# Optimization experiments

Measured on AMD Instinct MI355X. Metric: run time of the kernel, lower is better.

The kernel has to match this reference:

```python
import jax, jax.numpy as jnp
import numpy as np

K_NN = 16  # number of nearest neighbors (module init arg k)


def setup_inputs() -> dict:
    key = jax.random.key(0)
    k1, k2 = jax.random.split(key)
    xyz = jax.random.normal(k1, (8, 16384, 3), dtype=jnp.float32)
    centers = jax.random.normal(k2, (8, 1024, 3), dtype=jnp.float32)
    return {"xyz": xyz, "centers": centers}


def reference(xyz, centers):
    # avoiding the (B, N, K, 3) broadcast intermediate of the original while
    # computing the same torch.norm(xyz - centers, dim=-1) math.
    x_sq = jnp.sum(xyz * xyz, axis=-1)          # (B, N)
    c_sq = jnp.sum(centers * centers, axis=-1)  # (B, K)
    cross = jnp.einsum('bnd,bkd->bnk', xyz, centers)  # (B, N, K)
    d2 = x_sq[:, :, None] + c_sq[None if False else slice(None), None, :] - 2.0 * cross
    dist = jnp.sqrt(jnp.maximum(d2, 0.0))       # (B, N, K)
    # torch.topk(dist, k, dim=1, largest=False, sorted=True):
    # smallest-k over the N (points) axis, per center.
    neg = -jnp.transpose(dist, (0, 2, 1))       # (B, K, N)
    _, idx = jax.lax.top_k(neg, K_NN)           # (B, K, k), ascending distance
    return jnp.transpose(idx, (0, 2, 1))        # (B, k, K) to match torch dim=1 topk
```

## Files before the change

kernel.cpp:

```cpp
#include <hip/hip_runtime.h>
#include <stdint.h>

#define BB    8
#define NN    16384
#define KK    1024
#define KNN   16
#define CPB   8
#define WPB   8
#define EGRP  (NN / 4 / WPB)
#define PGRP  128
#define TCAP  256

typedef unsigned long long u64;

__device__ __forceinline__ u64 shfl_xor_u64(u64 v, int mask) {
    int lo = (int)(uint32_t)v;
    int hi = (int)(uint32_t)(v >> 32);
    lo = __shfl_xor(lo, mask, 64);
    hi = __shfl_xor(hi, mask, 64);
    return ((u64)(uint32_t)hi << 32) | (u64)(uint32_t)lo;
}

__device__ __forceinline__ u64 shfl_u64(u64 v, int src) {
    int lo = __shfl((int)(uint32_t)v, src, 64);
    int hi = __shfl((int)(uint32_t)(v >> 32), src, 64);
    return ((u64)(uint32_t)hi << 32) | (u64)(uint32_t)lo;
}

__device__ __forceinline__ u64 wave_min_u64(u64 v) {
#pragma unroll
    for (int off = 32; off > 0; off >>= 1) {
        u64 o = shfl_xor_u64(v, off);
        v = o < v ? o : v;
    }
    return v;
}

__device__ __forceinline__ void sort64_kv(u64& key, uint32_t& pay, int lane) {
#pragma unroll
    for (int k = 2; k <= 64; k <<= 1) {
#pragma unroll
        for (int j = k >> 1; j > 0; j >>= 1) {
            u64 okey = shfl_xor_u64(key, j);
            uint32_t opay = (uint32_t)__shfl_xor((int)pay, j, 64);
            bool tmin = ((lane & j) == 0) == ((lane & k) == 0);
            bool osm = okey < key;
            bool take = tmin ? osm : !osm;
            if (take) { key = okey; pay = opay; }
        }
    }
}

__device__ __forceinline__ void sort64_k(u64& key, int lane) {
#pragma unroll
    for (int k = 2; k <= 64; k <<= 1) {
#pragma unroll
        for (int j = k >> 1; j > 0; j >>= 1) {
            u64 okey = shfl_xor_u64(key, j);
            bool tmin = ((lane & j) == 0) == ((lane & k) == 0);
            bool osm = okey < key;
            bool take = tmin ? osm : !osm;
            if (take) key = okey;
        }
    }
}

__device__ __forceinline__ float point_d2(const float* xb, int i,
                                          float c0, float c1, float c2, float csq) {
#pragma clang fp contract(off)
    float x0 = xb[i * 3 + 0];
    float x1 = xb[i * 3 + 1];
    float x2 = xb[i * 3 + 2];
    float xsq = (x0 * x0 + x1 * x1) + x2 * x2;
    float cross = __fmaf_rn(x2, c2, __fmaf_rn(x1, c1, x0 * c0));
    float d2 = (xsq + csq) - 2.0f * cross;
    return d2 < 0.0f ? 0.0f : d2;
}

__device__ __attribute__((noinline)) int fallback_scan(const float* xb,
                                                       float c0, float c1, float c2,
                                                       float csq, int lane) {
    u64 list[KNN];
#pragma unroll
    for (int j = 0; j < KNN; ++j) list[j] = ~0ull;
    for (int i = lane; i < NN; i += 64) {
        float d2 = point_d2(xb, i, c0, c1, c2, csq);
        float dist = __fsqrt_rn(d2);
        u64 key = ((u64)__float_as_uint(dist) << 32) | (u64)(uint32_t)i;
        if (key < list[KNN - 1]) {
#pragma unroll
            for (int j = 0; j < KNN; ++j) {
                bool lt = key < list[j];
                u64 lo = lt ? key : list[j];
                u64 hi = lt ? list[j] : key;
                list[j] = lo;
                key = hi;
            }
        }
    }
    int res = 0;
    for (int it = 0; it < KNN; ++it) {
        u64 best = wave_min_u64(list[0]);
        if (it == lane) res = (int)(uint32_t)best;
        if (list[0] == best) {
#pragma unroll
            for (int j = 0; j < KNN - 1; ++j) list[j] = list[j + 1];
            list[KNN - 1] = ~0ull;
        }
    }
    return res;
}

__device__ __forceinline__ float sixteenth_smallest(float m, int lane) {
    uint32_t u = __float_as_uint(m);
    uint32_t s = (u & 0x80000000u) ? ~u : (u | 0x80000000u);
    u64 v = ((u64)s << 32) | (unsigned)lane;
#pragma unroll
    for (int k = 2; k <= 64; k <<= 1) {
#pragma unroll
        for (int j = k >> 1; j > 0; j >>= 1) {
            u64 o = shfl_xor_u64(v, j);
            bool up = (lane & k) == 0;
            bool takeMin = ((lane & j) == 0) == up;
            u64 mn = v < o ? v : o;
            u64 mx = v < o ? o : v;
            v = takeMin ? mn : mx;
        }
    }
    uint32_t sb = (uint32_t)__shfl((int)(uint32_t)(v >> 32), 15, 64);
    uint32_t ub = (sb & 0x80000000u) ? (sb ^ 0x80000000u) : ~sb;
    return __uint_as_float(ub);
}

__device__ __forceinline__ void load_group(const float4* x4, int g,
                                           float (&px)[4], float (&py)[4],
                                           float (&pz)[4], float (&xs)[4]) {
#pragma clang fp contract(off)
    float4 f0 = x4[g * 3 + 0];
    float4 f1 = x4[g * 3 + 1];
    float4 f2 = x4[g * 3 + 2];
    px[0] = f0.x; py[0] = f0.y; pz[0] = f0.z;
    px[1] = f0.w; py[1] = f1.x; pz[1] = f1.y;
    px[2] = f1.z; py[2] = f1.w; pz[2] = f2.x;
    px[3] = f2.y; py[3] = f2.z; pz[3] = f2.w;
#pragma unroll
    for (int k = 0; k < 4; ++k)
        xs[k] = (px[k] * px[k] + py[k] * py[k]) + pz[k] * pz[k];
}

__global__ __launch_bounds__(512, 4) void knn_kernel(const float* __restrict__ xyz,
                                                     const float* __restrict__ centers,
                                                     int* __restrict__ out) {
#pragma clang fp contract(off)
    const int q = (int)(threadIdx.x >> 6);
    const int lane = (int)(threadIdx.x & 63);
    const int cbase = (int)blockIdx.x * CPB;
    const int b = cbase >> 10;

    __shared__ float    s_min[CPB][512];
    __shared__ float    s_T[CPB];
    __shared__ int      s_cnt[CPB];
    __shared__ uint32_t s_idx[CPB][TCAP];

    float n[CPB][3];
#pragma unroll
    for (int c = 0; c < CPB; ++c) {
        n[c][0] = -2.0f * centers[(cbase + c) * 3 + 0];
        n[c][1] = -2.0f * centers[(cbase + c) * 3 + 1];
        n[c][2] = -2.0f * centers[(cbase + c) * 3 + 2];
    }

    const float* xb = xyz + (size_t)b * NN * 3;
    const float4* x4 = (const float4*)xb;
    const int gbase = q * EGRP;

    float m[CPB];
#pragma unroll
    for (int c = 0; c < CPB; ++c) m[c] = __builtin_inff();
#pragma unroll
    for (int s = 0; s < PGRP / 64; ++s) {
        int g = gbase + s * 64 + lane;
        float px[4], py[4], pz[4], xs[4];
        load_group(x4, g, px, py, pz, xs);
#pragma unroll
        for (int k = 0; k < 4; ++k) {
#pragma unroll
            for (int c = 0; c < CPB; ++c) {
                float d = __fmaf_rn(px[k], n[c][0],
                          __fmaf_rn(py[k], n[c][1],
                          __fmaf_rn(pz[k], n[c][2], xs[k])));
                m[c] = d < m[c] ? d : m[c];
            }
        }
    }
#pragma unroll
    for (int c = 0; c < CPB; ++c) s_min[c][threadIdx.x] = m[c];
    if (threadIdx.x < CPB) s_cnt[threadIdx.x] = 0;
    __syncthreads();
    {
        float v = s_min[q][lane];
#pragma unroll
        for (int w = 1; w < WPB; ++w) v = fminf(v, s_min[q][w * 64 + lane]);
        float t = sixteenth_smallest(v, lane);
        if (lane == 0) s_T[q] = t;
    }
    __syncthreads();
    float U[CPB];
#pragma unroll
    for (int c = 0; c < CPB; ++c) {
        float T = s_T[c];
        U[c] = T + fabsf(T) * 1e-5f + 5e-4f;
    }

#pragma unroll 2
    for (int s = 0; s < EGRP / 64; ++s) {
        int g = gbase + s * 64 + lane;
        float px[4], py[4], pz[4], xs[4];
        load_group(x4, g, px, py, pz, xs);
#pragma unroll
        for (int k = 0; k < 4; ++k) {
            int i = g * 4 + k;
#pragma unroll
            for (int c = 0; c < CPB; ++c) {
                float d = __fmaf_rn(px[k], n[c][0],
                          __fmaf_rn(py[k], n[c][1],
                          __fmaf_rn(pz[k], n[c][2], xs[k])));
                if (d <= U[c]) {
                    int pos = atomicAdd(&s_cnt[c], 1);
                    if (pos < TCAP) s_idx[c][pos] = (uint32_t)i;
                }
            }
        }
    }
    __syncthreads();

    const int cc = cbase + q;
    const float c0 = centers[cc * 3 + 0];
    const float c1 = centers[cc * 3 + 1];
    const float c2 = centers[cc * 3 + 2];
    const float csq = (c0 * c0 + c1 * c1) + c2 * c2;
    const int total = s_cnt[q];

    uint32_t outIdx;
    if (total <= TCAP) {
        u64 l0 = ~0ull, l1 = ~0ull, l2 = ~0ull, l3 = ~0ull;
        for (int j = lane; j < total; j += 64) {
            int idx = (int)s_idx[q][j];
            float d2 = point_d2(xb, idx, c0, c1, c2, csq);
            u64 key = ((u64)__float_as_uint(__fsqrt_rn(d2)) << 32) | (u64)(uint32_t)idx;
            bool t;
            t = key < l0; { u64 lo = t ? key : l0, hi = t ? l0 : key; l0 = lo; key = hi; }
            t = key < l1; { u64 lo = t ? key : l1, hi = t ? l1 : key; l1 = lo; key = hi; }
            t = key < l2; { u64 lo = t ? key : l2, hi = t ? l2 : key; l2 = lo; key = hi; }
            t = key < l3; { u64 lo = t ? key : l3, hi = t ? l3 : key; l3 = lo; key = hi; }
        }
        u64 key = l0;
        uint32_t pay = (uint32_t)lane;
        sort64_kv(key, pay, lane);
        int pos = lane >> 2, elem = lane & 3;
        int sid = __shfl((int)pay, pos, 64);
        u64 g0 = shfl_u64(l0, sid);
        u64 g1 = shfl_u64(l1, sid);
        u64 g2 = shfl_u64(l2, sid);
        u64 g3 = shfl_u64(l3, sid);
        u64 gk = (elem == 0) ? g0 : (elem == 1) ? g1 : (elem == 2) ? g2 : g3;
        sort64_k(gk, lane);
        outIdx = (uint32_t)gk;
    } else {
        outIdx = (uint32_t)fallback_scan(xb, c0, c1, c2, csq, lane);
    }

    if (lane < KNN) {
        out[((size_t)b * KNN + lane) * KK + (cc & 1023)] = (int)outIdx;
    }
}

extern "C" void kernel_launch(void* const* d_in, const int* in_sizes, int n_in,
                              void* d_out, int out_size, void* d_ws, size_t ws_size,
                              hipStream_t stream) {
    const float* xyz = (const float*)d_in[0];
    const float* centers = (const float*)d_in[1];
    int* out = (int*)d_out;
    (void)d_ws; (void)ws_size;

    const int nblocks = BB * KK / CPB;
    hipLaunchKernelGGL(knn_kernel, dim3(nblocks), dim3(512), 0, stream,
                       xyz, centers, out);
}
```

Baseline: 103.8 us.

## Add SoA prep pass, packed FMA distances, and per-wave candidate buckets

Adds a prep kernel that converts xyz into a structure-of-arrays buffer holding x, y, z and the precomputed squared norms in workspace. The main kernel now computes distances with v_pk_fma_f32 on packed pairs. Blocks shrink to 256 threads with 4 centers each, which doubles the grid. Candidate collection now uses a separate shared-memory counter per wave, to cut atomic contention. The trade-off is an extra kernel launch, extra global memory traffic for the SoA buffer, and each block rereading the points for fewer centers.

```diff
diff --git a/kernel.cpp b/kernel.cpp
--- a/kernel.cpp
+++ b/kernel.cpp
@@ -5,13 +5,21 @@
 #define NN    16384
 #define KK    1024
 #define KNN   16
-#define CPB   8
-#define WPB   8
-#define EGRP  (NN / 4 / WPB)
-#define PGRP  128
-#define TCAP  256
+#define QTR   (NN / 4)
+#define QGRP  (QTR / 4)
+#define PGRP  256
+#define HCAP  96
+#define NGRP_TOT (BB * NN / 4)
 
 typedef unsigned long long u64;
+typedef float f32x2 __attribute__((ext_vector_type(2)));
+typedef float f32x4 __attribute__((ext_vector_type(4)));
+
+__device__ __forceinline__ f32x2 pk_fma(f32x2 a, f32x2 b, f32x2 c) {
+    f32x2 d;
+    asm("v_pk_fma_f32 %0, %1, %2, %3" : "=v"(d) : "v"(a), "v"(b), "v"(c));
+    return d;
+}
 
 __device__ __forceinline__ u64 shfl_xor_u64(u64 v, int mask) {
     int lo = (int)(uint32_t)v;
@@ -148,87 +156,137 @@
         xs[k] = (px[k] * px[k] + py[k] * py[k]) + pz[k] * pz[k];
 }
 
-__global__ __launch_bounds__(512, 4) void knn_kernel(const float* __restrict__ xyz,
+__global__ __launch_bounds__(256) void prep_kernel(const float* __restrict__ xyz,
+                                                   float* __restrict__ soa) {
+#pragma clang fp contract(off)
+    int g = (int)blockIdx.x * 256 + (int)threadIdx.x;
+    const float4* x4 = (const float4*)xyz;
+    float px[4], py[4], pz[4], xs[4];
+    load_group(x4, g, px, py, pz, xs);
+    int b = g >> 12;
+    int gl = g & 4095;
+    f32x4* out4 = (f32x4*)(soa + (size_t)b * NN * 4);
+    out4[gl]          = f32x4{px[0], px[1], px[2], px[3]};
+    out4[4096  + gl]  = f32x4{py[0], py[1], py[2], py[3]};
+    out4[8192  + gl]  = f32x4{pz[0], pz[1], pz[2], pz[3]};
+    out4[12288 + gl]  = f32x4{xs[0], xs[1], xs[2], xs[3]};
+}
+
+template<bool SOA>
+__global__ __launch_bounds__(256, 6) void knn_kernel(const float* __restrict__ xyz,
                                                      const float* __restrict__ centers,
+                                                     const float* __restrict__ soa,
                                                      int* __restrict__ out) {
 #pragma clang fp contract(off)
     const int q = (int)(threadIdx.x >> 6);
     const int lane = (int)(threadIdx.x & 63);
-    const int cbase = (int)blockIdx.x * CPB;
+    const int cbase = (int)blockIdx.x * 4;
     const int b = cbase >> 10;
 
-    __shared__ float    s_min[CPB][512];
-    __shared__ float    s_T[CPB];
-    __shared__ int      s_cnt[CPB];
-    __shared__ uint32_t s_idx[CPB][TCAP];
-
-    float n[CPB][3];
-#pragma unroll
-    for (int c = 0; c < CPB; ++c) {
-        n[c][0] = -2.0f * centers[(cbase + c) * 3 + 0];
-        n[c][1] = -2.0f * centers[(cbase + c) * 3 + 1];
-        n[c][2] = -2.0f * centers[(cbase + c) * 3 + 2];
+    __shared__ float    s_min[4][256];
+    __shared__ float    s_T[4];
+    __shared__ int      s_cnt[4][4];
+    __shared__ uint32_t s_idx[4][4][HCAP];
+
+    f32x2 nx[4], ny[4], nz[4];
+#pragma unroll
+    for (int c = 0; c < 4; ++c) {
+        float a0 = -2.0f * centers[(cbase + c) * 3 + 0];
+        float a1 = -2.0f * centers[(cbase + c) * 3 + 1];
+        float a2 = -2.0f * centers[(cbase + c) * 3 + 2];
+        nx[c] = f32x2{a0, a0};
+        ny[c] = f32x2{a1, a1};
+        nz[c] = f32x2{a2, a2};
     }
 
     const float* xb = xyz + (size_t)b * NN * 3;
     const float4* x4 = (const float4*)xb;
-    const int gbase = q * EGRP;
-
-    float m[CPB];
-#pragma unroll
-    for (int c = 0; c < CPB; ++c) m[c] = __builtin_inff();
-#pragma unroll
+    const f32x4* sb4 = (const f32x4*)(soa + (size_t)b * NN * 4);
+    const int gbase = q * QGRP;
+
+    auto load_pairs = [&](int g, f32x2& xl, f32x2& xh, f32x2& yl, f32x2& yh,
+                          f32x2& zl, f32x2& zh, f32x2& sl, f32x2& sh) {
+        if constexpr (SOA) {
+            f32x4 X = sb4[g];
+            f32x4 Y = sb4[4096 + g];
+            f32x4 Z = sb4[8192 + g];
+            f32x4 S = sb4[12288 + g];
+            xl = __builtin_shufflevector(X, X, 0, 1);
+            xh = __builtin_shufflevector(X, X, 2, 3);
+            yl = __builtin_shufflevector(Y, Y, 0, 1);
+            yh = __builtin_shufflevector(Y, Y, 2, 3);
+            zl = __builtin_shufflevector(Z, Z, 0, 1);
+            zh = __builtin_shufflevector(Z, Z, 2, 3);
+            sl = __builtin_shufflevector(S, S, 0, 1);
+            sh = __builtin_shufflevector(S, S, 2, 3);
+        } else {
+            float px[4], py[4], pz[4], xs[4];
+            load_group(x4, g, px, py, pz, xs);
+            xl = f32x2{px[0], px[1]}; xh = f32x2{px[2], px[3]};
+            yl = f32x2{py[0], py[1]}; yh = f32x2{py[2], py[3]};
+            zl = f32x2{pz[0], pz[1]}; zh = f32x2{pz[2], pz[3]};
+            sl = f32x2{xs[0], xs[1]}; sh = f32x2{xs[2], xs[3]};
+        }
+    };
+
+    float m[4];
+#pragma unroll
+    for (int c = 0; c < 4; ++c) m[c] = __builtin_inff();
+#pragma unroll 2
     for (int s = 0; s < PGRP / 64; ++s) {
         int g = gbase + s * 64 + lane;
-        float px[4], py[4], pz[4], xs[4];
-        load_group(x4, g, px, py, pz, xs);
-#pragma unroll
-        for (int k = 0; k < 4; ++k) {
-#pragma unroll
-            for (int c = 0; c < CPB; ++c) {
-                float d = __fmaf_rn(px[k], n[c][0],
-                          __fmaf_rn(py[k], n[c][1],
-                          __fmaf_rn(pz[k], n[c][2], xs[k])));
-                m[c] = d < m[c] ? d : m[c];
-            }
-        }
-    }
-#pragma unroll
-    for (int c = 0; c < CPB; ++c) s_min[c][threadIdx.x] = m[c];
-    if (threadIdx.x < CPB) s_cnt[threadIdx.x] = 0;
+        f32x2 xl, xh, yl, yh, zl, zh, sl, sh;
+        load_pairs(g, xl, xh, yl, yh, zl, zh, sl, sh);
+#pragma unroll
+        for (int c = 0; c < 4; ++c) {
+            f32x2 dl = pk_fma(xl, nx[c], pk_fma(yl, ny[c], pk_fma(zl, nz[c], sl)));
+            f32x2 dh = pk_fma(xh, nx[c], pk_fma(yh, ny[c], pk_fma(zh, nz[c], sh)));
+            m[c] = fminf(m[c], fminf(fminf(dl.x, dl.y), fminf(dh.x, dh.y)));
+        }
+    }
+#pragma unroll
+    for (int c = 0; c < 4; ++c) s_min[c][threadIdx.x] = m[c];
+    if (threadIdx.x < 16) s_cnt[threadIdx.x >> 2][threadIdx.x & 3] = 0;
     __syncthreads();
     {
-        float v = s_min[q][lane];
-#pragma unroll
-        for (int w = 1; w < WPB; ++w) v = fminf(v, s_min[q][w * 64 + lane]);
+        float v = fminf(fminf(s_min[q][lane], s_min[q][64 + lane]),
+                        fminf(s_min[q][128 + lane], s_min[q][192 + lane]));
         float t = sixteenth_smallest(v, lane);
         if (lane == 0) s_T[q] = t;
     }
     __syncthreads();
-    float U[CPB];
-#pragma unroll
-    for (int c = 0; c < CPB; ++c) {
+    float U[4];
+#pragma unroll
+    for (int c = 0; c < 4; ++c) {
         float T = s_T[c];
         U[c] = T + fabsf(T) * 1e-5f + 5e-4f;
     }
 
 #pragma unroll 2
-    for (int s = 0; s < EGRP / 64; ++s) {
+    for (int s = 0; s < QGRP / 64; ++s) {
         int g = gbase + s * 64 + lane;
-        float px[4], py[4], pz[4], xs[4];
-        load_group(x4, g, px, py, pz, xs);
-#pragma unroll
-        for (int k = 0; k < 4; ++k) {
-            int i = g * 4 + k;
-#pragma unroll
-            for (int c = 0; c < CPB; ++c) {
-                float d = __fmaf_rn(px[k], n[c][0],
-                          __fmaf_rn(py[k], n[c][1],
-                          __fmaf_rn(pz[k], n[c][2], xs[k])));
-                if (d <= U[c]) {
-                    int pos = atomicAdd(&s_cnt[c], 1);
-                    if (pos < TCAP) s_idx[c][pos] = (uint32_t)i;
-                }
+        f32x2 xl, xh, yl, yh, zl, zh, sl, sh;
+        load_pairs(g, xl, xh, yl, yh, zl, zh, sl, sh);
+        int ibase = g * 4;
+#pragma unroll
+        for (int c = 0; c < 4; ++c) {
+            f32x2 dl = pk_fma(xl, nx[c], pk_fma(yl, ny[c], pk_fma(zl, nz[c], sl)));
+            f32x2 dh = pk_fma(xh, nx[c], pk_fma(yh, ny[c], pk_fma(zh, nz[c], sh)));
+            if (dl.x <= U[c]) {
+                int pos = atomicAdd(&s_cnt[c][q], 1);
+                if (pos < HCAP) s_idx[c][q][pos] = (uint32_t)(ibase + 0);
+            }
+            if (dl.y <= U[c]) {
+                int pos = atomicAdd(&s_cnt[c][q], 1);
+                if (pos < HCAP) s_idx[c][q][pos] = (uint32_t)(ibase + 1);
+            }
+            if (dh.x <= U[c]) {
+                int pos = atomicAdd(&s_cnt[c][q], 1);
+                if (pos < HCAP) s_idx[c][q][pos] = (uint32_t)(ibase + 2);
+            }
+            if (dh.y <= U[c]) {
+                int pos = atomicAdd(&s_cnt[c][q], 1);
+                if (pos < HCAP) s_idx[c][q][pos] = (uint32_t)(ibase + 3);
             }
         }
     }
@@ -239,13 +297,22 @@
     const float c1 = centers[cc * 3 + 1];
     const float c2 = centers[cc * 3 + 2];
     const float csq = (c0 * c0 + c1 * c1) + c2 * c2;
-    const int total = s_cnt[q];
-
-    uint32_t outIdx;
-    if (total <= TCAP) {
+    const int k0 = s_cnt[q][0], k1 = s_cnt[q][1], k2 = s_cnt[q][2], k3 = s_cnt[q][3];
+    const int p1o = k0, p2o = k0 + k1, p3o = k0 + k1 + k2;
+    const int total = p3o + k3;
+    const bool ok = (k0 <= HCAP) & (k1 <= HCAP) & (k2 <= HCAP) & (k3 <= HCAP) &
+                    (total <= 4 * 64);
+
+    uint32_t res;
+    if (ok) {
         u64 l0 = ~0ull, l1 = ~0ull, l2 = ~0ull, l3 = ~0ull;
         for (int j = lane; j < total; j += 64) {
-            int idx = (int)s_idx[q][j];
+            int qq, off;
+            if (j < p1o)      { qq = 0; off = j; }
+            else if (j < p2o) { qq = 1; off = j - p1o; }
+            else if (j < p3o) { qq = 2; off = j - p2o; }
+            else              { qq = 3; off = j - p3o; }
+            int idx = (int)s_idx[q][qq][off];
             float d2 = point_d2(xb, idx, c0, c1, c2, csq);
             u64 key = ((u64)__float_as_uint(__fsqrt_rn(d2)) << 32) | (u64)(uint32_t)idx;
             bool t;
@@ -265,13 +332,13 @@
         u64 g3 = shfl_u64(l3, sid);
         u64 gk = (elem == 0) ? g0 : (elem == 1) ? g1 : (elem == 2) ? g2 : g3;
         sort64_k(gk, lane);
-        outIdx = (uint32_t)gk;
+        res = (uint32_t)gk;
     } else {
-        outIdx = (uint32_t)fallback_scan(xb, c0, c1, c2, csq, lane);
+        res = (uint32_t)fallback_scan(xb, c0, c1, c2, csq, lane);
     }
 
     if (lane < KNN) {
-        out[((size_t)b * KNN + lane) * KK + (cc & 1023)] = (int)outIdx;
+        out[((size_t)b * KNN + lane) * KK + (cc & 1023)] = (int)res;
     }
 }
 
@@ -281,9 +348,16 @@
     const float* xyz = (const float*)d_in[0];
     const float* centers = (const float*)d_in[1];
     int* out = (int*)d_out;
-    (void)d_ws; (void)ws_size;
-
-    const int nblocks = BB * KK / CPB;
-    hipLaunchKernelGGL(knn_kernel, dim3(nblocks), dim3(512), 0, stream,
-                       xyz, centers, out);
-}
+
+    const int nblocks = BB * KK / 4;
+    const size_t need = (size_t)BB * NN * 4 * sizeof(float);
+    if (d_ws != nullptr && ws_size >= need) {
+        hipLaunchKernelGGL(prep_kernel, dim3(NGRP_TOT / 256), dim3(256), 0, stream,
+                           xyz, (float*)d_ws);
+        hipLaunchKernelGGL((knn_kernel<true>), dim3(nblocks), dim3(256), 0, stream,
+                           xyz, centers, (const float*)d_ws, out);
+    } else {
+        hipLaunchKernelGGL((knn_kernel<false>), dim3(nblocks), dim3(256), 0, stream,
+                           xyz, centers, (const float*)nullptr, out);
+    }
+}
```

Result: slower. 112.8 us (+8.6%).
